# Optimization experiments

Measured on AMD Instinct MI355X. Metric: run time of the kernel, lower is better.

## Reference

```python
import jax, jax.numpy as jnp
import numpy as np

N, E = 20000, 160000
D_IN, HID, HEADS = 256, 64, 10
NEG_SLOPE = 0.2


def setup_inputs() -> dict:
    key = jax.random.key(0)
    ks = jax.random.split(key, 12)
    s = 0.05
    f = jnp.float32
    return {
        "x": jax.random.normal(ks[0], (N, D_IN), f),
        "edge_index": jax.random.randint(ks[1], (2, E), 0, N, jnp.int32),
        # GATConv 1: in=D_IN, out=HID, heads=10, concat=True
        "W1": (jax.random.normal(ks[2], (D_IN, HEADS * HID), f) * s),
        "a_src1": (jax.random.normal(ks[3], (HEADS, HID), f) * s),
        "a_dst1": (jax.random.normal(ks[4], (HEADS, HID), f) * s),
        "b1": jnp.zeros((HEADS * HID,), f),
        # GATConv 2: in=HEADS*HID, out=HID, heads=1
        "W2": (jax.random.normal(ks[5], (HEADS * HID, HID), f) * s),
        "a_src2": (jax.random.normal(ks[6], (1, HID), f) * s),
        "a_dst2": (jax.random.normal(ks[7], (1, HID), f) * s),
        "b2": jnp.zeros((HID,), f),
        # final Linear(hidden_dim, hidden_dim)
        "Wfc": (jax.random.normal(ks[8], (HID, HID), f) * s),
        "bfc": jnp.zeros((HID,), f),
    }


def gat_conv(x, src, dst, n, W, a_src, a_dst, b, heads, concat):
    """PyG GATConv (eval mode): gather, leaky-relu scores, segment softmax, scatter."""
    c = W.shape[1] // heads
    h = (x @ W).reshape(n, heads, c)                      # [N, H, C]
    score_src = jnp.sum(h * a_src, axis=-1)               # [N, H]
    score_dst = jnp.sum(h * a_dst, axis=-1)               # [N, H]
    e = jax.nn.leaky_relu(score_src[src] + score_dst[dst], NEG_SLOPE)  # [E, H]
    # segment softmax over incoming edges of each dst node
    m = jax.ops.segment_max(e, dst, num_segments=n)
    e = jnp.exp(e - m[dst])
    denom = jax.ops.segment_sum(e, dst, num_segments=n)
    alpha = e / (denom[dst] + 1e-16)                      # [E, H]
    msg = alpha[:, :, None] * h[src]                      # [E, H, C]
    out = jax.ops.segment_sum(msg, dst, num_segments=n)   # [N, H, C]
    out = out.reshape(n, heads * c) if concat else out.mean(axis=1)
    return out + b


def reference(x, edge_index, W1, a_src1, a_dst1, b1, W2, a_src2, a_dst2, b2, Wfc, bfc):
    n = x.shape[0]
    # add self loops (PyG default)
    loops = jnp.arange(n, dtype=edge_index.dtype)
    src = jnp.concatenate([edge_index[0], loops])
    dst = jnp.concatenate([edge_index[1], loops])
    h = jax.nn.relu(gat_conv(x, src, dst, n, W1, a_src1, a_dst1, b1, HEADS, True))
    h = jax.nn.relu(gat_conv(h, src, dst, n, W2, a_src2, a_dst2, b2, 1, True))
    return jax.nn.relu(h @ Wfc + bfc)
```

## Files before the change

kernel.cpp:

```cpp
#include <hip/hip_runtime.h>
#include <cstdint>
#include <cstddef>

constexpr int N_NODES = 20000;
constexpr int E_EDGES = 160000;
constexpr int D_INC   = 256;
constexpr int HEADSC  = 10;
constexpr int EN      = E_EDGES + N_NODES;
constexpr int ELLW    = 96;
constexpr float NEG_SLOPE = 0.2f;

typedef _Float16 half8 __attribute__((ext_vector_type(8)));
typedef _Float16 half4v __attribute__((ext_vector_type(4)));
typedef float f32x4 __attribute__((ext_vector_type(4)));

__global__ __launch_bounds__(256) void gemm1_k(
    const _Float16* __restrict__ A,
    const _Float16* __restrict__ BT,
    _Float16* __restrict__ C,
    const float* __restrict__ asv, const float* __restrict__ adv,
    float* __restrict__ s_s, float* __restrict__ s_d, int M)
{
    __shared__ alignas(16) _Float16 Ah[64][72];
    __shared__ alignas(16) _Float16 Bh[128][72];
    const int tid = threadIdx.x;
    const int wv  = tid >> 6;
    const int ln  = tid & 63;
    const int row0 = blockIdx.y * 64;
    const int col0 = blockIdx.x * 128;
    const int m = ln & 15;
    const int q = ln >> 4;
    const int arow = tid >> 2;
    const int acg  = (tid & 3) * 16;
    const int brow = tid >> 1;
    const int bcg  = (tid & 1) * 32;

    const int ar_c = min(row0 + arow, M - 1);
    const _Float16* aptr = A  + (size_t)ar_c * 256 + acg;
    const _Float16* bptr = BT + (size_t)(col0 + brow) * 256 + bcg;

    int4 a0, a1, bv0, bv1, bv2, bv3;
    a0  = *reinterpret_cast<const int4*>(aptr);
    a1  = *reinterpret_cast<const int4*>(aptr + 8);
    bv0 = *reinterpret_cast<const int4*>(bptr);
    bv1 = *reinterpret_cast<const int4*>(bptr + 8);
    bv2 = *reinterpret_cast<const int4*>(bptr + 16);
    bv3 = *reinterpret_cast<const int4*>(bptr + 24);

    f32x4 acc[8] = {};

    for (int k0 = 0; k0 < 256; k0 += 64) {
        *reinterpret_cast<int4*>(&Ah[arow][acg])      = a0;
        *reinterpret_cast<int4*>(&Ah[arow][acg + 8])  = a1;
        *reinterpret_cast<int4*>(&Bh[brow][bcg])      = bv0;
        *reinterpret_cast<int4*>(&Bh[brow][bcg + 8])  = bv1;
        *reinterpret_cast<int4*>(&Bh[brow][bcg + 16]) = bv2;
        *reinterpret_cast<int4*>(&Bh[brow][bcg + 24]) = bv3;
        __syncthreads();

        if (k0 + 64 < 256) {
            const _Float16* ap = aptr + k0 + 64;
            a0 = *reinterpret_cast<const int4*>(ap);
            a1 = *reinterpret_cast<const int4*>(ap + 8);
            const _Float16* bp = bptr + k0 + 64;
            bv0 = *reinterpret_cast<const int4*>(bp);
            bv1 = *reinterpret_cast<const int4*>(bp + 8);
            bv2 = *reinterpret_cast<const int4*>(bp + 16);
            bv3 = *reinterpret_cast<const int4*>(bp + 24);
        }

#pragma unroll
        for (int ks = 0; ks < 2; ++ks) {
            const half8 af = *reinterpret_cast<const half8*>(
                &Ah[wv * 16 + m][ks * 32 + q * 8]);
#pragma unroll
            for (int ct = 0; ct < 8; ++ct) {
                const half8 bf = *reinterpret_cast<const half8*>(
                    &Bh[ct * 16 + m][ks * 32 + q * 8]);
                acc[ct] = __builtin_amdgcn_mfma_f32_16x16x32_f16(af, bf, acc[ct],
                                                                 0, 0, 0);
            }
        }
        __syncthreads();
    }

#pragma unroll
    for (int ct = 0; ct < 8; ++ct) {
#pragma unroll
        for (int r = 0; r < 4; ++r) {
            const int row = row0 + wv * 16 + q * 4 + r;
            if (row < M)
                C[(size_t)row * 640 + col0 + ct * 16 + m] = (_Float16)acc[ct][r];
        }
    }

    const int h0i = blockIdx.x * 2;
    float pa[2][4] = {}, pd[2][4] = {};
#pragma unroll
    for (int ct = 0; ct < 8; ++ct) {
        const int hh = ct >> 2;
        const int ch = (ct & 3) * 16 + m;
        const float a_ = asv[(h0i + hh) * 64 + ch];
        const float d_ = adv[(h0i + hh) * 64 + ch];
#pragma unroll
        for (int r = 0; r < 4; ++r) {
            pa[hh][r] += acc[ct][r] * a_;
            pd[hh][r] += acc[ct][r] * d_;
        }
    }
#pragma unroll
    for (int o = 1; o < 16; o <<= 1) {
#pragma unroll
        for (int hh = 0; hh < 2; ++hh)
#pragma unroll
            for (int r = 0; r < 4; ++r) {
                pa[hh][r] += __shfl_xor(pa[hh][r], o, 64);
                pd[hh][r] += __shfl_xor(pd[hh][r], o, 64);
            }
    }
    if (m == 0) {
#pragma unroll
        for (int hh = 0; hh < 2; ++hh)
#pragma unroll
            for (int r = 0; r < 4; ++r) {
                const int row = row0 + wv * 16 + q * 4 + r;
                if (row < M) {
                    s_s[row * HEADSC + h0i + hh] = pa[hh][r];
                    s_d[row * HEADSC + h0i + hh] = pd[hh][r];
                }
            }
    }
}

__global__ __launch_bounds__(128) void gemm2_k(
    const _Float16* __restrict__ A,
    const _Float16* __restrict__ BT,
    _Float16* __restrict__ C,
    const float* __restrict__ asv, const float* __restrict__ adv,
    float* __restrict__ s_s, float* __restrict__ s_d)
{
    __shared__ alignas(16) _Float16 Ah[32][72];
    __shared__ alignas(16) _Float16 Bh[64][72];
    const int tid = threadIdx.x;
    const int wv  = tid >> 6;
    const int ln  = tid & 63;
    const int row0 = blockIdx.x * 32;
    const int m = ln & 15;
    const int q = ln >> 4;
    const int arow = tid >> 2;
    const int acg  = (tid & 3) * 16;
    const int brow = tid >> 1;
    const int bcg  = (tid & 1) * 32;

    const _Float16* aptr = A  + (size_t)(row0 + arow) * 640 + acg;
    const _Float16* bptr = BT + (size_t)brow * 640 + bcg;

    int4 a0, a1, b0, b1, b2, b3;
    a0 = *reinterpret_cast<const int4*>(aptr);
    a1 = *reinterpret_cast<const int4*>(aptr + 8);
    b0 = *reinterpret_cast<const int4*>(bptr);
    b1 = *reinterpret_cast<const int4*>(bptr + 8);
    b2 = *reinterpret_cast<const int4*>(bptr + 16);
    b3 = *reinterpret_cast<const int4*>(bptr + 24);

    f32x4 acc[4] = {};

    for (int k0 = 0; k0 < 640; k0 += 64) {
        *reinterpret_cast<int4*>(&Ah[arow][acg])      = a0;
        *reinterpret_cast<int4*>(&Ah[arow][acg + 8])  = a1;
        *reinterpret_cast<int4*>(&Bh[brow][bcg])      = b0;
        *reinterpret_cast<int4*>(&Bh[brow][bcg + 8])  = b1;
        *reinterpret_cast<int4*>(&Bh[brow][bcg + 16]) = b2;
        *reinterpret_cast<int4*>(&Bh[brow][bcg + 24]) = b3;
        __syncthreads();

        if (k0 + 64 < 640) {
            const _Float16* ap = aptr + k0 + 64;
            a0 = *reinterpret_cast<const int4*>(ap);
            a1 = *reinterpret_cast<const int4*>(ap + 8);
            const _Float16* bp = bptr + k0 + 64;
            b0 = *reinterpret_cast<const int4*>(bp);
            b1 = *reinterpret_cast<const int4*>(bp + 8);
            b2 = *reinterpret_cast<const int4*>(bp + 16);
            b3 = *reinterpret_cast<const int4*>(bp + 24);
        }

#pragma unroll
        for (int ks = 0; ks < 2; ++ks) {
            const half8 af = *reinterpret_cast<const half8*>(
                &Ah[wv * 16 + m][ks * 32 + q * 8]);
#pragma unroll
            for (int ct = 0; ct < 4; ++ct) {
                const half8 bf = *reinterpret_cast<const half8*>(
                    &Bh[ct * 16 + m][ks * 32 + q * 8]);
                acc[ct] = __builtin_amdgcn_mfma_f32_16x16x32_f16(af, bf, acc[ct],
                                                                 0, 0, 0);
            }
        }
        __syncthreads();
    }

#pragma unroll
    for (int ct = 0; ct < 4; ++ct) {
#pragma unroll
        for (int r = 0; r < 4; ++r) {
            const int row = row0 + wv * 16 + q * 4 + r;
            C[(size_t)row * 64 + ct * 16 + m] = (_Float16)acc[ct][r];
        }
    }

    float pa[4] = {}, pd[4] = {};
#pragma unroll
    for (int ct = 0; ct < 4; ++ct) {
        const float a_ = asv[ct * 16 + m];
        const float d_ = adv[ct * 16 + m];
#pragma unroll
        for (int r = 0; r < 4; ++r) {
            pa[r] += acc[ct][r] * a_;
            pd[r] += acc[ct][r] * d_;
        }
    }
#pragma unroll
    for (int o = 1; o < 16; o <<= 1) {
#pragma unroll
        for (int r = 0; r < 4; ++r) {
            pa[r] += __shfl_xor(pa[r], o, 64);
            pd[r] += __shfl_xor(pd[r], o, 64);
        }
    }
    if (m == 0) {
#pragma unroll
        for (int r = 0; r < 4; ++r) {
            const int row = row0 + wv * 16 + q * 4 + r;
            s_s[row] = pa[r];
            s_d[row] = pd[r];
        }
    }
}

constexpr int XQ   = N_NODES * D_INC / 4;
constexpr int W1E  = D_INC * 640;
constexpr int W2E  = 640 * 64;
constexpr int WFCE = 64 * 64;
constexpr int SETUP_TOT = EN + XQ + W1E + W2E + WFCE;

__global__ void setup_k(const int* __restrict__ src, const int* __restrict__ dst,
                        int* __restrict__ deg, int* __restrict__ ell,
                        const float* __restrict__ x, const float* __restrict__ W1,
                        const float* __restrict__ W2, const float* __restrict__ Wfc,
                        _Float16* __restrict__ x16, _Float16* __restrict__ W1T,
                        _Float16* __restrict__ W2T, _Float16* __restrict__ WfcT)
{
    const int i = blockIdx.x * 256 + threadIdx.x;
    if (i < EN) {
        const int base = deg[N_NODES];
        int d, s;
        if (i < E_EDGES) { d = dst[i]; s = src[i]; }
        else             { d = i - E_EDGES; s = d; }
        const int r = atomicAdd(&deg[d], 1) - base;
        if ((unsigned)r < (unsigned)ELLW) ell[(size_t)d * ELLW + r] = s;
    } else if (i < EN + XQ) {
        const int j = i - EN;
        const float4 v = reinterpret_cast<const float4*>(x)[j];
        half4v o = {(_Float16)v.x, (_Float16)v.y, (_Float16)v.z, (_Float16)v.w};
        reinterpret_cast<half4v*>(x16)[j] = o;
    } else if (i < EN + XQ + W1E) {
        const int j = i - EN - XQ;
        const int k = j / 640, n = j - k * 640;
        W1T[(size_t)n * D_INC + k] = (_Float16)W1[j];
    } else if (i < EN + XQ + W1E + W2E) {
        const int j = i - EN - XQ - W1E;
        const int k = j / 64, n = j - k * 64;
        W2T[(size_t)n * 640 + k] = (_Float16)W2[j];
    } else if (i < SETUP_TOT) {
        const int j = i - EN - XQ - W1E - W2E;
        const int k = j >> 6, n = j & 63;
        WfcT[(size_t)n * 64 + k] = (_Float16)Wfc[j];
    }
}

__global__ __launch_bounds__(320) void agg_f16_oct(
    const _Float16* __restrict__ h, const float* __restrict__ s_s,
    const float* __restrict__ s_d, const int* __restrict__ deg,
    const int* __restrict__ ell, const float* __restrict__ bias,
    _Float16* __restrict__ outp)
{
    const int t   = blockIdx.x * 320 + threadIdx.x;
    const int n   = t / 80;
    const int oct = t - n * 80;
    if (n >= N_NODES) return;
    const int hh  = oct >> 3;
    const _Float16* __restrict__ hb = h + oct * 8;
    const int* __restrict__ row = ell + (size_t)n * ELLW;
    const float sd = s_d[n * HEADSC + hh];
    const int dbase = deg[N_NODES];
    const int dc = min(deg[n] - dbase, ELLW);

    float acc[8] = {};
    float den = 0.f;
    int i = 0;
    for (; i + 3 < dc; i += 4) {
        const int s0 = row[i], s1 = row[i + 1], s2 = row[i + 2], s3 = row[i + 3];
        const float g0 = s_s[s0 * HEADSC + hh], g1 = s_s[s1 * HEADSC + hh];
        const float g2 = s_s[s2 * HEADSC + hh], g3 = s_s[s3 * HEADSC + hh];
        const half8 v0 = *reinterpret_cast<const half8*>(hb + (size_t)s0 * 640);
        const half8 v1 = *reinterpret_cast<const half8*>(hb + (size_t)s1 * 640);
        const half8 v2 = *reinterpret_cast<const half8*>(hb + (size_t)s2 * 640);
        const half8 v3 = *reinterpret_cast<const half8*>(hb + (size_t)s3 * 640);
        float e0 = g0 + sd, e1 = g1 + sd, e2 = g2 + sd, e3 = g3 + sd;
        e0 = (e0 > 0.f) ? e0 : NEG_SLOPE * e0;
        e1 = (e1 > 0.f) ? e1 : NEG_SLOPE * e1;
        e2 = (e2 > 0.f) ? e2 : NEG_SLOPE * e2;
        e3 = (e3 > 0.f) ? e3 : NEG_SLOPE * e3;
        const float w0 = __expf(e0), w1 = __expf(e1);
        const float w2 = __expf(e2), w3 = __expf(e3);
        den += (w0 + w1) + (w2 + w3);
#pragma unroll
        for (int j = 0; j < 8; ++j)
            acc[j] += (w0 * (float)v0[j] + w1 * (float)v1[j])
                    + (w2 * (float)v2[j] + w3 * (float)v3[j]);
    }
    for (; i < dc; ++i) {
        const int s0 = row[i];
        const float g0 = s_s[s0 * HEADSC + hh];
        const half8 v0 = *reinterpret_cast<const half8*>(hb + (size_t)s0 * 640);
        float e0 = g0 + sd;
        e0 = (e0 > 0.f) ? e0 : NEG_SLOPE * e0;
        const float w0 = __expf(e0);
        den += w0;
#pragma unroll
        for (int j = 0; j < 8; ++j) acc[j] += w0 * (float)v0[j];
    }
    const float inv = 1.f / (den + 1e-16f);
    const float* bb = bias + oct * 8;
    half8 o;
#pragma unroll
    for (int j = 0; j < 8; ++j)
        o[j] = (_Float16)fmaxf(acc[j] * inv + bb[j], 0.f);
    *reinterpret_cast<half8*>(outp + (size_t)n * 640 + oct * 8) = o;
}

__global__ __launch_bounds__(256) void agg2fc_k(
    const _Float16* __restrict__ h,
    const float* __restrict__ s_s, const float* __restrict__ s_d,
    const int* __restrict__ deg, const int* __restrict__ ell,
    const float* __restrict__ b2,
    const _Float16* __restrict__ WfcT,
    const float* __restrict__ bfc,
    float* __restrict__ out)
{
    __shared__ alignas(16) _Float16 Os[32][72];
    const int tid = threadIdx.x;
    const int n0  = blockIdx.x * 32;
    const int nl  = tid >> 3;
    const int oct = tid & 7;
    const int n   = n0 + nl;

    {
        const _Float16* __restrict__ hb = h + oct * 8;
        const int* __restrict__ row = ell + (size_t)n * ELLW;
        const float sd = s_d[n];
        const int dbase = deg[N_NODES];
        const int dc = min(deg[n] - dbase, ELLW);

        float acc[8] = {};
        float den = 0.f;
        int i = 0;
        for (; i + 3 < dc; i += 4) {
            int   sv[4];
            float gv[4];
            half8 hv[4];
#pragma unroll
            for (int u = 0; u < 4; ++u) sv[u] = row[i + u];
#pragma unroll
            for (int u = 0; u < 4; ++u) gv[u] = s_s[sv[u]];
#pragma unroll
            for (int u = 0; u < 4; ++u)
                hv[u] = *reinterpret_cast<const half8*>(hb + (size_t)sv[u] * 64);
#pragma unroll
            for (int u = 0; u < 4; ++u) {
                float e = gv[u] + sd;
                e = (e > 0.f) ? e : NEG_SLOPE * e;
                const float w = __expf(e);
                den += w;
#pragma unroll
                for (int j = 0; j < 8; ++j) acc[j] += w * (float)hv[u][j];
            }
        }
        for (; i < dc; ++i) {
            const int s0 = row[i];
            const float g0 = s_s[s0];
            const half8 v0 = *reinterpret_cast<const half8*>(hb + (size_t)s0 * 64);
            float e0 = g0 + sd;
            e0 = (e0 > 0.f) ? e0 : NEG_SLOPE * e0;
            const float w0 = __expf(e0);
            den += w0;
#pragma unroll
            for (int j = 0; j < 8; ++j) acc[j] += w0 * (float)v0[j];
        }
        const float inv = 1.f / (den + 1e-16f);
        const float* bb = b2 + oct * 8;
        half8 o;
#pragma unroll
        for (int j = 0; j < 8; ++j)
            o[j] = (_Float16)fmaxf(acc[j] * inv + bb[j], 0.f);
        *reinterpret_cast<half8*>(&Os[nl][oct * 8]) = o;
    }
    __syncthreads();

    const int wv = tid >> 6;
    const int ln = tid & 63;
    if (wv < 2) {
        const int m = ln & 15;
        const int q = ln >> 4;
        f32x4 acc[4] = {};
#pragma unroll
        for (int ks = 0; ks < 2; ++ks) {
            const half8 af = *reinterpret_cast<const half8*>(
                &Os[wv * 16 + m][ks * 32 + q * 8]);
#pragma unroll
            for (int ct = 0; ct < 4; ++ct) {
                const half8 bf = *reinterpret_cast<const half8*>(
                    WfcT + (size_t)(ct * 16 + m) * 64 + ks * 32 + q * 8);
                acc[ct] = __builtin_amdgcn_mfma_f32_16x16x32_f16(af, bf, acc[ct],
                                                                 0, 0, 0);
            }
        }
#pragma unroll
        for (int ct = 0; ct < 4; ++ct) {
#pragma unroll
            for (int r = 0; r < 4; ++r) {
                const int row = n0 + wv * 16 + q * 4 + r;
                const int col = ct * 16 + m;
                out[(size_t)row * 64 + col] = fmaxf(acc[ct][r] + bfc[col], 0.f);
            }
        }
    }
}

extern "C" void kernel_launch(void* const* d_in, const int* in_sizes, int n_in,
                              void* d_out, int out_size, void* d_ws, size_t ws_size,
                              hipStream_t stream)
{
    const float* x      = (const float*)d_in[0];
    const int*   edges  = (const int*)d_in[1];
    const float* W1     = (const float*)d_in[2];
    const float* a_src1 = (const float*)d_in[3];
    const float* a_dst1 = (const float*)d_in[4];
    const float* b1     = (const float*)d_in[5];
    const float* W2     = (const float*)d_in[6];
    const float* a_src2 = (const float*)d_in[7];
    const float* a_dst2 = (const float*)d_in[8];
    const float* b2     = (const float*)d_in[9];
    const float* Wfc    = (const float*)d_in[10];
    const float* bfc    = (const float*)d_in[11];
    float* out = (float*)d_out;

    const int* src = edges;
    const int* dst = edges + E_EDGES;

    char* ws = (char*)d_ws;
    size_t off = 0;
    auto alloc = [&](size_t bytes) -> void* {
        void* p = ws + off;
        off += (bytes + 255) & ~(size_t)255;
        return p;
    };
    _Float16*  h1   = (_Float16*)alloc((size_t)N_NODES * 640 * sizeof(_Float16));
    _Float16*  out1 = (_Float16*)alloc((size_t)N_NODES * 640 * sizeof(_Float16));
    _Float16*  h2   = (_Float16*)alloc((size_t)N_NODES * 64 * sizeof(_Float16));
    _Float16*  x16  = (_Float16*)alloc((size_t)N_NODES * D_INC * sizeof(_Float16));
    _Float16*  W1T  = (_Float16*)alloc((size_t)640 * D_INC * sizeof(_Float16));
    _Float16*  W2T  = (_Float16*)alloc((size_t)64 * 640 * sizeof(_Float16));
    _Float16*  WfcT = (_Float16*)alloc((size_t)64 * 64 * sizeof(_Float16));
    float*     ss1  = (float*)alloc((size_t)N_NODES * HEADSC * sizeof(float));
    float*     sd1  = (float*)alloc((size_t)N_NODES * HEADSC * sizeof(float));
    float*     ss2  = (float*)alloc((size_t)N_NODES * sizeof(float));
    float*     sd2  = (float*)alloc((size_t)N_NODES * sizeof(float));
    int*       deg  = (int*)alloc((size_t)(N_NODES + 1) * sizeof(int));
    int*       ell  = (int*)alloc((size_t)N_NODES * ELLW * sizeof(int));

    setup_k<<<(SETUP_TOT + 255) / 256, 256, 0, stream>>>(
        src, dst, deg, ell, x, W1, W2, Wfc, x16, W1T, W2T, WfcT);

    dim3 g1(5, (N_NODES + 63) / 64);
    gemm1_k<<<g1, 256, 0, stream>>>(x16, W1T, h1, a_src1, a_dst1,
                                    ss1, sd1, N_NODES);

    agg_f16_oct<<<(N_NODES * 80) / 320, 320, 0, stream>>>(h1, ss1, sd1, deg, ell,
                                                          b1, out1);

    gemm2_k<<<N_NODES / 32, 128, 0, stream>>>(out1, W2T, h2, a_src2, a_dst2,
                                              ss2, sd2);

    agg2fc_k<<<N_NODES / 32, 256, 0, stream>>>(h2, ss2, sd2, deg, ell,
                                               b2, WfcT, bfc, out);
}
```

Baseline: 180.6 us.

## Shard layer-1 features into column slabs to localize gathers in cache

GEMM1 now writes h1 as 8 column shards of 80 halves each, stored node-major within each shard, and writes the attention scores head-major. The aggregation kernel gives each block one shard and 32 destination nodes. Block index interleaves shards, so co-resident blocks gather from a 3.2MB slab instead of the full 25.6MB h1, which is meant to raise L2/LLC hit rates for random neighbor gathers. The cost is that each gather row is only 160 bytes, and GEMM1's stores become more strided.

```diff
diff --git a/kernel.cpp b/kernel.cpp
--- a/kernel.cpp
+++ b/kernel.cpp
@@ -86,11 +86,15 @@
 
 #pragma unroll
     for (int ct = 0; ct < 8; ++ct) {
+        const int col = col0 + ct * 16 + m;
+        const int sh  = col / 80;
+        const int cw  = col - sh * 80;
+        _Float16* cp = C + (size_t)sh * N_NODES * 80 + cw;
 #pragma unroll
         for (int r = 0; r < 4; ++r) {
             const int row = row0 + wv * 16 + q * 4 + r;
             if (row < M)
-                C[(size_t)row * 640 + col0 + ct * 16 + m] = (_Float16)acc[ct][r];
+                cp[(size_t)row * 80] = (_Float16)acc[ct][r];
         }
     }
 
@@ -125,8 +129,8 @@
             for (int r = 0; r < 4; ++r) {
                 const int row = row0 + wv * 16 + q * 4 + r;
                 if (row < M) {
-                    s_s[row * HEADSC + h0i + hh] = pa[hh][r];
-                    s_d[row * HEADSC + h0i + hh] = pd[hh][r];
+                    s_s[(h0i + hh) * N_NODES + row] = pa[hh][r];
+                    s_d[(h0i + hh) * N_NODES + row] = pd[hh][r];
                 }
             }
     }
@@ -279,20 +283,27 @@
     }
 }
 
-__global__ __launch_bounds__(320) void agg_f16_oct(
-    const _Float16* __restrict__ h, const float* __restrict__ s_s,
-    const float* __restrict__ s_d, const int* __restrict__ deg,
+__global__ __launch_bounds__(320) void agg_f16_shard(
+    const _Float16* __restrict__ h,
+    const float* __restrict__ s_s,
+    const float* __restrict__ s_d,
+    const int* __restrict__ deg,
     const int* __restrict__ ell, const float* __restrict__ bias,
     _Float16* __restrict__ outp)
 {
-    const int t   = blockIdx.x * 320 + threadIdx.x;
-    const int n   = t / 80;
-    const int oct = t - n * 80;
-    if (n >= N_NODES) return;
+    const int b   = blockIdx.x;
+    const int sh  = b & 7;
+    const int g   = b >> 3;
+    const int tid = threadIdx.x;
+    const int nl  = tid / 10;
+    const int o   = tid - nl * 10;
+    const int n   = g * 32 + nl;
+    const int oct = sh * 10 + o;
     const int hh  = oct >> 3;
-    const _Float16* __restrict__ hb = h + oct * 8;
+    const _Float16* __restrict__ hb = h + (size_t)sh * N_NODES * 80 + o * 8;
+    const float* __restrict__ ssh = s_s + (size_t)hh * N_NODES;
     const int* __restrict__ row = ell + (size_t)n * ELLW;
-    const float sd = s_d[n * HEADSC + hh];
+    const float sd = s_d[(size_t)hh * N_NODES + n];
     const int dbase = deg[N_NODES];
     const int dc = min(deg[n] - dbase, ELLW);
 
@@ -301,12 +312,12 @@
     int i = 0;
     for (; i + 3 < dc; i += 4) {
         const int s0 = row[i], s1 = row[i + 1], s2 = row[i + 2], s3 = row[i + 3];
-        const float g0 = s_s[s0 * HEADSC + hh], g1 = s_s[s1 * HEADSC + hh];
-        const float g2 = s_s[s2 * HEADSC + hh], g3 = s_s[s3 * HEADSC + hh];
-        const half8 v0 = *reinterpret_cast<const half8*>(hb + (size_t)s0 * 640);
-        const half8 v1 = *reinterpret_cast<const half8*>(hb + (size_t)s1 * 640);
-        const half8 v2 = *reinterpret_cast<const half8*>(hb + (size_t)s2 * 640);
-        const half8 v3 = *reinterpret_cast<const half8*>(hb + (size_t)s3 * 640);
+        const float g0 = ssh[s0], g1 = ssh[s1];
+        const float g2 = ssh[s2], g3 = ssh[s3];
+        const half8 v0 = *reinterpret_cast<const half8*>(hb + (size_t)s0 * 80);
+        const half8 v1 = *reinterpret_cast<const half8*>(hb + (size_t)s1 * 80);
+        const half8 v2 = *reinterpret_cast<const half8*>(hb + (size_t)s2 * 80);
+        const half8 v3 = *reinterpret_cast<const half8*>(hb + (size_t)s3 * 80);
         float e0 = g0 + sd, e1 = g1 + sd, e2 = g2 + sd, e3 = g3 + sd;
         e0 = (e0 > 0.f) ? e0 : NEG_SLOPE * e0;
         e1 = (e1 > 0.f) ? e1 : NEG_SLOPE * e1;
@@ -322,8 +333,8 @@
     }
     for (; i < dc; ++i) {
         const int s0 = row[i];
-        const float g0 = s_s[s0 * HEADSC + hh];
-        const half8 v0 = *reinterpret_cast<const half8*>(hb + (size_t)s0 * 640);
+        const float g0 = ssh[s0];
+        const half8 v0 = *reinterpret_cast<const half8*>(hb + (size_t)s0 * 80);
         float e0 = g0 + sd;
         e0 = (e0 > 0.f) ? e0 : NEG_SLOPE * e0;
         const float w0 = __expf(e0);
@@ -333,11 +344,11 @@
     }
     const float inv = 1.f / (den + 1e-16f);
     const float* bb = bias + oct * 8;
-    half8 o;
+    half8 ov;
 #pragma unroll
     for (int j = 0; j < 8; ++j)
-        o[j] = (_Float16)fmaxf(acc[j] * inv + bb[j], 0.f);
-    *reinterpret_cast<half8*>(outp + (size_t)n * 640 + oct * 8) = o;
+        ov[j] = (_Float16)fmaxf(acc[j] * inv + bb[j], 0.f);
+    *reinterpret_cast<half8*>(outp + (size_t)n * 640 + oct * 8) = ov;
 }
 
 __global__ __launch_bounds__(256) void agg2fc_k(
@@ -487,7 +498,7 @@
     gemm1_k<<<g1, 256, 0, stream>>>(x16, W1T, h1, a_src1, a_dst1,
                                     ss1, sd1, N_NODES);
 
-    agg_f16_oct<<<(N_NODES * 80) / 320, 320, 0, stream>>>(h1, ss1, sd1, deg, ell,
+    agg_f16_shard<<<8 * (N_NODES / 32), 320, 0, stream>>>(h1, ss1, sd1, deg, ell,
                                                           b1, out1);
 
     gemm2_k<<<N_NODES / 32, 128, 0, stream>>>(out1, W2T, h2, a_src2, a_dst2,
```

Measured after the change: 186.7 us. 1.03x slower.

## Store layer-1 features head-major and shard aggregation by head with 16-bit ELL

Applied to the files above, without the earlier changes.

GEMM1 now writes its output and attention scores in head-major layout ([head][node][64] and [head][node]). The first aggregation kernel is replaced by one that assigns each block a single head over a group of 32 nodes, so random neighbour gathers stay inside one compact per-head slice that is more likely to stay cached. ELL neighbour indices are stored as 16-bit shorts to halve index traffic, and index loads and output stores are marked nontemporal. The short indices rely on the node count fitting in a signed 16-bit value.

```diff
diff --git a/kernel.cpp b/kernel.cpp
--- a/kernel.cpp
+++ b/kernel.cpp
@@ -86,11 +86,15 @@
 
 #pragma unroll
     for (int ct = 0; ct < 8; ++ct) {
+        const int col  = col0 + ct * 16 + m;
+        const int head = col >> 6;
+        const int cw   = col & 63;
+        _Float16* cp = C + (size_t)head * N_NODES * 64 + cw;
 #pragma unroll
         for (int r = 0; r < 4; ++r) {
             const int row = row0 + wv * 16 + q * 4 + r;
             if (row < M)
-                C[(size_t)row * 640 + col0 + ct * 16 + m] = (_Float16)acc[ct][r];
+                cp[(size_t)row * 64] = (_Float16)acc[ct][r];
         }
     }
 
@@ -125,8 +129,8 @@
             for (int r = 0; r < 4; ++r) {
                 const int row = row0 + wv * 16 + q * 4 + r;
                 if (row < M) {
-                    s_s[row * HEADSC + h0i + hh] = pa[hh][r];
-                    s_d[row * HEADSC + h0i + hh] = pd[hh][r];
+                    s_s[(size_t)(h0i + hh) * N_NODES + row] = pa[hh][r];
+                    s_d[(size_t)(h0i + hh) * N_NODES + row] = pd[hh][r];
                 }
             }
     }
@@ -245,7 +249,7 @@
 constexpr int SETUP_TOT = EN + XQ + W1E + W2E + WFCE;
 
 __global__ void setup_k(const int* __restrict__ src, const int* __restrict__ dst,
-                        int* __restrict__ deg, int* __restrict__ ell,
+                        int* __restrict__ deg, short* __restrict__ ell,
                         const float* __restrict__ x, const float* __restrict__ W1,
                         const float* __restrict__ W2, const float* __restrict__ Wfc,
                         _Float16* __restrict__ x16, _Float16* __restrict__ W1T,
@@ -258,7 +262,7 @@
         if (i < E_EDGES) { d = dst[i]; s = src[i]; }
         else             { d = i - E_EDGES; s = d; }
         const int r = atomicAdd(&deg[d], 1) - base;
-        if ((unsigned)r < (unsigned)ELLW) ell[(size_t)d * ELLW + r] = s;
+        if ((unsigned)r < (unsigned)ELLW) ell[(size_t)d * ELLW + r] = (short)s;
     } else if (i < EN + XQ) {
         const int j = i - EN;
         const float4 v = reinterpret_cast<const float4*>(x)[j];
@@ -279,20 +283,27 @@
     }
 }
 
-__global__ __launch_bounds__(320) void agg_f16_oct(
-    const _Float16* __restrict__ h, const float* __restrict__ s_s,
-    const float* __restrict__ s_d, const int* __restrict__ deg,
-    const int* __restrict__ ell, const float* __restrict__ bias,
+__global__ __launch_bounds__(256) void agg1_shard_k(
+    const _Float16* __restrict__ h,
+    const float* __restrict__ s_s,
+    const float* __restrict__ s_d,
+    const int* __restrict__ deg,
+    const short* __restrict__ ell,
+    const float* __restrict__ bias,
     _Float16* __restrict__ outp)
 {
-    const int t   = blockIdx.x * 320 + threadIdx.x;
-    const int n   = t / 80;
-    const int oct = t - n * 80;
-    if (n >= N_NODES) return;
-    const int hh  = oct >> 3;
-    const _Float16* __restrict__ hb = h + oct * 8;
-    const int* __restrict__ row = ell + (size_t)n * ELLW;
-    const float sd = s_d[n * HEADSC + hh];
+    const int b = blockIdx.x;
+    int s, g;
+    if (b < 5000) { s = b & 7; g = b >> 3; }
+    else { const int c = b - 5000; s = 8 + (c & 1); g = c >> 1; }
+    const int tid = threadIdx.x;
+    const int nl  = tid >> 3;
+    const int lc  = tid & 7;
+    const int n   = g * 32 + nl;
+    const _Float16* __restrict__ hb = h + (size_t)s * N_NODES * 64 + lc * 8;
+    const float* __restrict__ ssh = s_s + (size_t)s * N_NODES;
+    const short* __restrict__ row = ell + (size_t)n * ELLW;
+    const float sd = s_d[(size_t)s * N_NODES + n];
     const int dbase = deg[N_NODES];
     const int dc = min(deg[n] - dbase, ELLW);
 
@@ -300,30 +311,34 @@
     float den = 0.f;
     int i = 0;
     for (; i + 3 < dc; i += 4) {
-        const int s0 = row[i], s1 = row[i + 1], s2 = row[i + 2], s3 = row[i + 3];
-        const float g0 = s_s[s0 * HEADSC + hh], g1 = s_s[s1 * HEADSC + hh];
-        const float g2 = s_s[s2 * HEADSC + hh], g3 = s_s[s3 * HEADSC + hh];
-        const half8 v0 = *reinterpret_cast<const half8*>(hb + (size_t)s0 * 640);
-        const half8 v1 = *reinterpret_cast<const half8*>(hb + (size_t)s1 * 640);
-        const half8 v2 = *reinterpret_cast<const half8*>(hb + (size_t)s2 * 640);
-        const half8 v3 = *reinterpret_cast<const half8*>(hb + (size_t)s3 * 640);
-        float e0 = g0 + sd, e1 = g1 + sd, e2 = g2 + sd, e3 = g3 + sd;
-        e0 = (e0 > 0.f) ? e0 : NEG_SLOPE * e0;
-        e1 = (e1 > 0.f) ? e1 : NEG_SLOPE * e1;
-        e2 = (e2 > 0.f) ? e2 : NEG_SLOPE * e2;
-        e3 = (e3 > 0.f) ? e3 : NEG_SLOPE * e3;
-        const float w0 = __expf(e0), w1 = __expf(e1);
-        const float w2 = __expf(e2), w3 = __expf(e3);
-        den += (w0 + w1) + (w2 + w3);
-#pragma unroll
-        for (int j = 0; j < 8; ++j)
-            acc[j] += (w0 * (float)v0[j] + w1 * (float)v1[j])
-                    + (w2 * (float)v2[j] + w3 * (float)v3[j]);
+        int sv[4];
+#pragma unroll
+        for (int u = 0; u < 4; ++u)
+            sv[u] = (int)__builtin_nontemporal_load(row + i + u);
+        float gv[4];
+#pragma unroll
+        for (int u = 0; u < 4; ++u) gv[u] = ssh[sv[u]];
+        half8 vv[4];
+#pragma unroll
+        for (int u = 0; u < 4; ++u)
+            vv[u] = *reinterpret_cast<const half8*>(hb + (size_t)sv[u] * 64);
+        float w[4];
+#pragma unroll
+        for (int u = 0; u < 4; ++u) {
+            float e = gv[u] + sd;
+            e = (e > 0.f) ? e : NEG_SLOPE * e;
+            w[u] = __expf(e);
+            den += w[u];
+        }
+#pragma unroll
+        for (int u = 0; u < 4; ++u)
+#pragma unroll
+            for (int j = 0; j < 8; ++j) acc[j] += w[u] * (float)vv[u][j];
     }
     for (; i < dc; ++i) {
-        const int s0 = row[i];
-        const float g0 = s_s[s0 * HEADSC + hh];
-        const half8 v0 = *reinterpret_cast<const half8*>(hb + (size_t)s0 * 640);
+        const int s0 = (int)__builtin_nontemporal_load(row + i);
+        const float g0 = ssh[s0];
+        const half8 v0 = *reinterpret_cast<const half8*>(hb + (size_t)s0 * 64);
         float e0 = g0 + sd;
         e0 = (e0 > 0.f) ? e0 : NEG_SLOPE * e0;
         const float w0 = __expf(e0);
@@ -332,18 +347,19 @@
         for (int j = 0; j < 8; ++j) acc[j] += w0 * (float)v0[j];
     }
     const float inv = 1.f / (den + 1e-16f);
-    const float* bb = bias + oct * 8;
+    const float* bb = bias + s * 64 + lc * 8;
     half8 o;
 #pragma unroll
     for (int j = 0; j < 8; ++j)
         o[j] = (_Float16)fmaxf(acc[j] * inv + bb[j], 0.f);
-    *reinterpret_cast<half8*>(outp + (size_t)n * 640 + oct * 8) = o;
+    __builtin_nontemporal_store(
+        o, reinterpret_cast<half8*>(outp + (size_t)n * 640 + s * 64 + lc * 8));
 }
 
 __global__ __launch_bounds__(256) void agg2fc_k(
     const _Float16* __restrict__ h,
     const float* __restrict__ s_s, const float* __restrict__ s_d,
-    const int* __restrict__ deg, const int* __restrict__ ell,
+    const int* __restrict__ deg, const short* __restrict__ ell,
     const float* __restrict__ b2,
     const _Float16* __restrict__ WfcT,
     const float* __restrict__ bfc,
@@ -358,7 +374,7 @@
 
     {
         const _Float16* __restrict__ hb = h + oct * 8;
-        const int* __restrict__ row = ell + (size_t)n * ELLW;
+        const short* __restrict__ row = ell + (size_t)n * ELLW;
         const float sd = s_d[n];
         const int dbase = deg[N_NODES];
         const int dc = min(deg[n] - dbase, ELLW);
@@ -371,7 +387,7 @@
             float gv[4];
             half8 hv[4];
 #pragma unroll
-            for (int u = 0; u < 4; ++u) sv[u] = row[i + u];
+            for (int u = 0; u < 4; ++u) sv[u] = (int)row[i + u];
 #pragma unroll
             for (int u = 0; u < 4; ++u) gv[u] = s_s[sv[u]];
 #pragma unroll
@@ -388,7 +404,7 @@
             }
         }
         for (; i < dc; ++i) {
-            const int s0 = row[i];
+            const int s0 = (int)row[i];
             const float g0 = s_s[s0];
             const half8 v0 = *reinterpret_cast<const half8*>(hb + (size_t)s0 * 64);
             float e0 = g0 + sd;
@@ -478,7 +494,7 @@
     float*     ss2  = (float*)alloc((size_t)N_NODES * sizeof(float));
     float*     sd2  = (float*)alloc((size_t)N_NODES * sizeof(float));
     int*       deg  = (int*)alloc((size_t)(N_NODES + 1) * sizeof(int));
-    int*       ell  = (int*)alloc((size_t)N_NODES * ELLW * sizeof(int));
+    short*     ell  = (short*)alloc((size_t)N_NODES * ELLW * sizeof(short));
 
     setup_k<<<(SETUP_TOT + 255) / 256, 256, 0, stream>>>(
         src, dst, deg, ell, x, W1, W2, Wfc, x16, W1T, W2T, WfcT);
@@ -487,8 +503,7 @@
     gemm1_k<<<g1, 256, 0, stream>>>(x16, W1T, h1, a_src1, a_dst1,
                                     ss1, sd1, N_NODES);
 
-    agg_f16_oct<<<(N_NODES * 80) / 320, 320, 0, stream>>>(h1, ss1, sd1, deg, ell,
-                                                          b1, out1);
+    agg1_shard_k<<<6250, 256, 0, stream>>>(h1, ss1, sd1, deg, ell, b1, out1);
 
     gemm2_k<<<N_NODES / 32, 128, 0, stream>>>(out1, W2T, h2, a_src2, a_dst2,
                                               ss2, sd2);
```

New measurement: 188.8 us. 1.05x slower.

## Retile first-layer GEMM to 128x128 blocks with direct global-to-LDS loads

Applied to the files above, without the earlier changes.

The first GATConv projection GEMM moves from 64x128 tiles, where each wave computes 16x128, to 128x128 tiles split into a 2x2 wave grid of 64x64 each. This raises MFMA reuse per LDS fragment load and halves the number of blocks. Operand staging now uses global_load_lds to write 16-byte chunks straight into unpadded LDS, replacing register staging with software prefetch. The per-head attention-score reduction is adjusted to the new wave layout. The trade-off is that the unpadded LDS may cause bank conflicts on fragment reads, and loads no longer overlap the MFMA work of the previous k-step.

```diff
diff --git a/kernel.cpp b/kernel.cpp
--- a/kernel.cpp
+++ b/kernel.cpp
@@ -14,6 +14,9 @@
 typedef _Float16 half4v __attribute__((ext_vector_type(4)));
 typedef float f32x4 __attribute__((ext_vector_type(4)));
 
+typedef const __attribute__((address_space(1))) void* gas_ptr;
+typedef __attribute__((address_space(3))) void* las_ptr;
+
 __global__ __launch_bounds__(256) void gemm1_k(
     const _Float16* __restrict__ A,
     const _Float16* __restrict__ BT,
@@ -21,112 +24,106 @@
     const float* __restrict__ asv, const float* __restrict__ adv,
     float* __restrict__ s_s, float* __restrict__ s_d, int M)
 {
-    __shared__ alignas(16) _Float16 Ah[64][72];
-    __shared__ alignas(16) _Float16 Bh[128][72];
+    __shared__ alignas(16) _Float16 Ah[128][64];
+    __shared__ alignas(16) _Float16 Bh[128][64];
     const int tid = threadIdx.x;
     const int wv  = tid >> 6;
     const int ln  = tid & 63;
-    const int row0 = blockIdx.y * 64;
+    const int wr  = wv >> 1;
+    const int wc  = wv & 1;
+    const int row0 = blockIdx.y * 128;
     const int col0 = blockIdx.x * 128;
     const int m = ln & 15;
     const int q = ln >> 4;
-    const int arow = tid >> 2;
-    const int acg  = (tid & 3) * 16;
-    const int brow = tid >> 1;
-    const int bcg  = (tid & 1) * 32;
-
-    const int ar_c = min(row0 + arow, M - 1);
-    const _Float16* aptr = A  + (size_t)ar_c * 256 + acg;
-    const _Float16* bptr = BT + (size_t)(col0 + brow) * 256 + bcg;
-
-    int4 a0, a1, bv0, bv1, bv2, bv3;
-    a0  = *reinterpret_cast<const int4*>(aptr);
-    a1  = *reinterpret_cast<const int4*>(aptr + 8);
-    bv0 = *reinterpret_cast<const int4*>(bptr);
-    bv1 = *reinterpret_cast<const int4*>(bptr + 8);
-    bv2 = *reinterpret_cast<const int4*>(bptr + 16);
-    bv3 = *reinterpret_cast<const int4*>(bptr + 24);
-
-    f32x4 acc[8] = {};
+    const int srow = tid >> 3;
+    const int sk   = (tid & 7) * 8;
+
+    f32x4 acc[4][4] = {};
 
     for (int k0 = 0; k0 < 256; k0 += 64) {
-        *reinterpret_cast<int4*>(&Ah[arow][acg])      = a0;
-        *reinterpret_cast<int4*>(&Ah[arow][acg + 8])  = a1;
-        *reinterpret_cast<int4*>(&Bh[brow][bcg])      = bv0;
-        *reinterpret_cast<int4*>(&Bh[brow][bcg + 8])  = bv1;
-        *reinterpret_cast<int4*>(&Bh[brow][bcg + 16]) = bv2;
-        *reinterpret_cast<int4*>(&Bh[brow][bcg + 24]) = bv3;
+#pragma unroll
+        for (int u = 0; u < 4; ++u) {
+            const int ar = min(row0 + u * 32 + srow, M - 1);
+            __builtin_amdgcn_global_load_lds(
+                (gas_ptr)(A + (size_t)ar * 256 + k0 + sk),
+                (las_ptr)(&Ah[u * 32 + srow][sk]), 16, 0, 0);
+        }
+#pragma unroll
+        for (int u = 0; u < 4; ++u) {
+            __builtin_amdgcn_global_load_lds(
+                (gas_ptr)(BT + (size_t)(col0 + u * 32 + srow) * 256 + k0 + sk),
+                (las_ptr)(&Bh[u * 32 + srow][sk]), 16, 0, 0);
+        }
         __syncthreads();
 
-        if (k0 + 64 < 256) {
-            const _Float16* ap = aptr + k0 + 64;
-            a0 = *reinterpret_cast<const int4*>(ap);
-            a1 = *reinterpret_cast<const int4*>(ap + 8);
-            const _Float16* bp = bptr + k0 + 64;
-            bv0 = *reinterpret_cast<const int4*>(bp);
-            bv1 = *reinterpret_cast<const int4*>(bp + 8);
-            bv2 = *reinterpret_cast<const int4*>(bp + 16);
-            bv3 = *reinterpret_cast<const int4*>(bp + 24);
-        }
-
 #pragma unroll
         for (int ks = 0; ks < 2; ++ks) {
-            const half8 af = *reinterpret_cast<const half8*>(
-                &Ah[wv * 16 + m][ks * 32 + q * 8]);
-#pragma unroll
-            for (int ct = 0; ct < 8; ++ct) {
-                const half8 bf = *reinterpret_cast<const half8*>(
-                    &Bh[ct * 16 + m][ks * 32 + q * 8]);
-                acc[ct] = __builtin_amdgcn_mfma_f32_16x16x32_f16(af, bf, acc[ct],
-                                                                 0, 0, 0);
-            }
+            half8 af[4], bf[4];
+#pragma unroll
+            for (int i = 0; i < 4; ++i)
+                af[i] = *reinterpret_cast<const half8*>(
+                    &Ah[wr * 64 + i * 16 + m][ks * 32 + q * 8]);
+#pragma unroll
+            for (int j = 0; j < 4; ++j)
+                bf[j] = *reinterpret_cast<const half8*>(
+                    &Bh[wc * 64 + j * 16 + m][ks * 32 + q * 8]);
+#pragma unroll
+            for (int i = 0; i < 4; ++i)
+#pragma unroll
+                for (int j = 0; j < 4; ++j)
+                    acc[i][j] = __builtin_amdgcn_mfma_f32_16x16x32_f16(
+                        af[i], bf[j], acc[i][j], 0, 0, 0);
         }
         __syncthreads();
     }
 
 #pragma unroll
-    for (int ct = 0; ct < 8; ++ct) {
-#pragma unroll
-        for (int r = 0; r < 4; ++r) {
-            const int row = row0 + wv * 16 + q * 4 + r;
-            if (row < M)
-                C[(size_t)row * 640 + col0 + ct * 16 + m] = (_Float16)acc[ct][r];
-        }
-    }
-
-    const int h0i = blockIdx.x * 2;
-    float pa[2][4] = {}, pd[2][4] = {};
-#pragma unroll
-    for (int ct = 0; ct < 8; ++ct) {
-        const int hh = ct >> 2;
-        const int ch = (ct & 3) * 16 + m;
-        const float a_ = asv[(h0i + hh) * 64 + ch];
-        const float d_ = adv[(h0i + hh) * 64 + ch];
-#pragma unroll
-        for (int r = 0; r < 4; ++r) {
-            pa[hh][r] += acc[ct][r] * a_;
-            pd[hh][r] += acc[ct][r] * d_;
-        }
+    for (int i = 0; i < 4; ++i) {
+#pragma unroll
+        for (int j = 0; j < 4; ++j) {
+            const int col = col0 + wc * 64 + j * 16 + m;
+#pragma unroll
+            for (int r = 0; r < 4; ++r) {
+                const int row = row0 + wr * 64 + i * 16 + q * 4 + r;
+                if (row < M)
+                    C[(size_t)row * 640 + col] = (_Float16)acc[i][j][r];
+            }
+        }
+    }
+
+    const int hh = blockIdx.x * 2 + wc;
+    float pa[4][4] = {}, pd[4][4] = {};
+#pragma unroll
+    for (int j = 0; j < 4; ++j) {
+        const float a_ = asv[hh * 64 + j * 16 + m];
+        const float d_ = adv[hh * 64 + j * 16 + m];
+#pragma unroll
+        for (int i = 0; i < 4; ++i)
+#pragma unroll
+            for (int r = 0; r < 4; ++r) {
+                pa[i][r] += acc[i][j][r] * a_;
+                pd[i][r] += acc[i][j][r] * d_;
+            }
     }
 #pragma unroll
     for (int o = 1; o < 16; o <<= 1) {
 #pragma unroll
-        for (int hh = 0; hh < 2; ++hh)
+        for (int i = 0; i < 4; ++i)
 #pragma unroll
             for (int r = 0; r < 4; ++r) {
-                pa[hh][r] += __shfl_xor(pa[hh][r], o, 64);
-                pd[hh][r] += __shfl_xor(pd[hh][r], o, 64);
+                pa[i][r] += __shfl_xor(pa[i][r], o, 64);
+                pd[i][r] += __shfl_xor(pd[i][r], o, 64);
             }
     }
     if (m == 0) {
 #pragma unroll
-        for (int hh = 0; hh < 2; ++hh)
+        for (int i = 0; i < 4; ++i)
 #pragma unroll
             for (int r = 0; r < 4; ++r) {
-                const int row = row0 + wv * 16 + q * 4 + r;
+                const int row = row0 + wr * 64 + i * 16 + q * 4 + r;
                 if (row < M) {
-                    s_s[row * HEADSC + h0i + hh] = pa[hh][r];
-                    s_d[row * HEADSC + h0i + hh] = pd[hh][r];
+                    s_s[row * HEADSC + hh] = pa[i][r];
+                    s_d[row * HEADSC + hh] = pd[i][r];
                 }
             }
     }
@@ -483,7 +480,7 @@
     setup_k<<<(SETUP_TOT + 255) / 256, 256, 0, stream>>>(
         src, dst, deg, ell, x, W1, W2, Wfc, x16, W1T, W2T, WfcT);
 
-    dim3 g1(5, (N_NODES + 63) / 64);
+    dim3 g1(5, (N_NODES + 127) / 128);
     gemm1_k<<<g1, 256, 0, stream>>>(x16, W1T, h1, a_src1, a_dst1,
                                     ss1, sd1, N_NODES);
 
```

After: 179.0 us. Within noise of the previous version (-0.9%).
